# Kernel tuning notes

Hardware: AMD Instinct MI355X
Metric: run time of the kernel (lower is better)

The kernel has to match this reference:

```python
import jax, jax.numpy as jnp
import numpy as np

HEADS = 4
DIM_HEAD = 32
EPS = 1e-5


def setup_inputs() -> dict:
    key = jax.random.key(0)
    ks = jax.random.split(key, 3)
    b, c, h, w = 32, 128, 128, 128
    hidden = HEADS * DIM_HEAD  # 128
    x = jax.random.normal(ks[0], (b, c, h, w), dtype=jnp.float32)
    Wqkv = jax.random.normal(ks[1], (3 * hidden, c), dtype=jnp.float32) * (1.0 / np.sqrt(c))
    Wout = jax.random.normal(ks[2], (c, hidden), dtype=jnp.float32) * (1.0 / np.sqrt(hidden))
    bout = jnp.zeros((c,), dtype=jnp.float32)
    g = jnp.ones((c,), dtype=jnp.float32)
    return {"x": x, "Wqkv": Wqkv, "Wout": Wout, "bout": bout, "g": g}


def reference(x, Wqkv, Wout, bout, g):
    b, c, h, w = x.shape
    n = h * w
    scale = DIM_HEAD ** -0.5
    # 1x1 conv (no bias) == channel GEMM
    qkv = jnp.einsum('oc,bchw->bohw', Wqkv, x)  # [b, 3*hidden, h, w]
    q, k, v = jnp.split(qkv, 3, axis=1)
    # b (h d) x y -> b h d n
    def to_heads(t):
        return t.reshape(b, HEADS, DIM_HEAD, n)
    q, k, v = to_heads(q), to_heads(k), to_heads(v)
    q = jax.nn.softmax(q, axis=-2) * scale   # softmax over per-head channel dim
    k = jax.nn.softmax(k, axis=-1)           # softmax over token dim
    v = v / n
    ctx = jnp.einsum('bhdn,bhen->bhde', k, v)   # [b, heads, d, e]
    out = jnp.einsum('bhde,bhdn->bhen', ctx, q)  # [b, heads, e, n]
    out = out.reshape(b, HEADS * DIM_HEAD, h, w)
    # output 1x1 conv with bias
    y = jnp.einsum('oc,bchw->bohw', Wout, out) + bout[None, :, None, None]
    # LayerNorm over channel dim (biased variance)
    mean = jnp.mean(y, axis=1, keepdims=True)
    var = jnp.var(y, axis=1, keepdims=True)
    return (y - mean) * jax.lax.rsqrt(var + EPS) * g[None, :, None, None]
```

## Files before the change

### kernel.cpp

```cpp
#include <hip/hip_runtime.h>
#include <math.h>


#define NCHUNK 64

typedef __attribute__((ext_vector_type(8))) short short8;
typedef __attribute__((ext_vector_type(4))) float f32x4;

__device__ __forceinline__ uint bf16r(float f) {
    uint u = __float_as_uint(f);
    return (u + 0x7FFFu + ((u >> 16) & 1u)) >> 16;
}
__device__ __forceinline__ float bf16f(uint h) { return __uint_as_float(h << 16); }
__device__ __forceinline__ uint2 bsplit(float f) {
    uint h = bf16r(f);
    float r = f - bf16f(h);
    return make_uint2(h, bf16r(r));
}
__device__ __forceinline__ uint2 bsplit_t(float f) {
    uint u = __float_as_uint(f);
    uint uh = u & 0xFFFF0000u;
    float r = f - __uint_as_float(uh);
    return make_uint2(uh >> 16, __float_as_uint(r) >> 16);
}
__device__ __forceinline__ uint bpack_t(float f) {
    uint u = __float_as_uint(f);
    uint uh = u & 0xFFFF0000u;
    float r = f - __uint_as_float(uh);
    return (uh >> 16) | (__float_as_uint(r) & 0xFFFF0000u);
}
__device__ __forceinline__ short8 lo8(uint4 a, uint4 b) {
    uint4 r;
    r.x = (a.x & 0xFFFFu) | (a.y << 16);
    r.y = (a.z & 0xFFFFu) | (a.w << 16);
    r.z = (b.x & 0xFFFFu) | (b.y << 16);
    r.w = (b.z & 0xFFFFu) | (b.w << 16);
    return __builtin_bit_cast(short8, r);
}
__device__ __forceinline__ short8 hi8(uint4 a, uint4 b) {
    uint4 r;
    r.x = (a.x >> 16) | (a.y & 0xFFFF0000u);
    r.y = (a.z >> 16) | (a.w & 0xFFFF0000u);
    r.z = (b.x >> 16) | (b.y & 0xFFFF0000u);
    r.w = (b.z >> 16) | (b.w & 0xFFFF0000u);
    return __builtin_bit_cast(short8, r);
}

__global__ __launch_bounds__(256)
void wsplit(const float* __restrict__ W, ushort* __restrict__ Wh,
            ushort* __restrict__ Wl, int n)
{
    const int base = (blockIdx.x * 256 + threadIdx.x) * 4;
    if (base + 3 < n) {
        const float4 f = *(const float4*)(W + base);
        const uint2 a = bsplit(f.x), b2 = bsplit(f.y), c = bsplit(f.z), d = bsplit(f.w);
        ushort4 hh; hh.x = (ushort)a.x; hh.y = (ushort)b2.x; hh.z = (ushort)c.x; hh.w = (ushort)d.x;
        ushort4 ll; ll.x = (ushort)a.y; ll.y = (ushort)b2.y; ll.z = (ushort)c.y; ll.w = (ushort)d.y;
        *(ushort4*)(Wh + base) = hh;
        *(ushort4*)(Wl + base) = ll;
    }
}

#define MFMA(A, B, C) __builtin_amdgcn_mfma_f32_16x16x32_bf16((A), (B), (C), 0, 0, 0)

__global__ __launch_bounds__(512, 1)
void la_k1(const float* __restrict__ x,
           const ushort* __restrict__ Wh, const ushort* __restrict__ Wl,
           float* __restrict__ Spart, float* __restrict__ Zpart)
{
    __shared__ __align__(16) char smb[163840];

    const int tid = threadIdx.x;
    const int b = blockIdx.y, chunk = blockIdx.x;
    const int w = tid >> 6, l = tid & 63;
    const int l15 = l & 15, lg = l >> 4;

    {
#pragma unroll
        for (int it = 0; it < 16; ++it) {
            const int q = tid + 512 * it;
            const int region = q >> 12;
            const int lin = (q & 4095) * 16;
            const int r = lin >> 8;
            const int dst = (region << 16) + (lin ^ ((r & 7) << 4));
            const ushort* src = (region ? Wl : Wh) + 128 * 128 + (lin >> 1);
            *(uint4*)(&smb[dst]) = *(const uint4*)src;
        }
    }

    f32x4 s2[2];
#pragma unroll
    for (int i = 0; i < 2; ++i) s2[i] = (f32x4){0.f, 0.f, 0.f, 0.f};
    float zrow[4];
#pragma unroll
    for (int i = 0; i < 4; ++i) zrow[i] = 0.f;

    const int hh = w >> 1, eh = w & 1;

    for (int t = 0; t < 8; ++t) {
        const int p0 = chunk * 256 + t * 32;
        {
            const float* xb = x + (size_t)b * 128 * 16384 + p0;
            const int cp = tid >> 3, j = tid & 7;
            const int pb = j * 4, c = cp * 2;
            const float4 a = *(const float4*)(xb + (size_t)c * 16384 + pb);
            const float4 bq = *(const float4*)(xb + (size_t)(c + 1) * 16384 + pb);
            const float av[4] = {a.x, a.y, a.z, a.w};
            const float bv[4] = {bq.x, bq.y, bq.z, bq.w};
#pragma unroll
            for (int pp = 0; pp < 4; ++pp) {
                const uint2 s0 = bsplit_t(av[pp]);
                const uint2 s1 = bsplit_t(bv[pp]);
                const int p = pb + pp;
                const int byt = (p * 256 + c * 2) ^ (((p ^ (p >> 3)) & 7) << 4);
                *(uint*)(&smb[131072 + byt])        = s0.x | (s1.x << 16);
                *(uint*)(&smb[131072 + 8192 + byt]) = s0.y | (s1.y << 16);
            }
        }
        __syncthreads();

        f32x4 acc[2][2];
#pragma unroll
        for (int rt = 0; rt < 2; ++rt)
#pragma unroll
            for (int ct = 0; ct < 2; ++ct) acc[rt][ct] = (f32x4){0.f, 0.f, 0.f, 0.f};
#pragma unroll
        for (int ks = 0; ks < 4; ++ks) {
            short8 Bh[2], Bl[2];
#pragma unroll
            for (int ct = 0; ct < 2; ++ct) {
                const int p = ct * 16 + l15;
                const int byt = (p * 256 + (ks * 32 + lg * 8) * 2) ^ (((p ^ (p >> 3)) & 7) << 4);
                Bh[ct] = *(const short8*)(&smb[131072 + byt]);
                Bl[ct] = *(const short8*)(&smb[131072 + 8192 + byt]);
            }
#pragma unroll
            for (int rt = 0; rt < 2; ++rt) {
                const int r = (w + rt * 8) * 16 + l15;
                const int abyt = (r * 256 + (ks * 32 + lg * 8) * 2) ^ ((r & 7) << 4);
                const short8 Ah_ = *(const short8*)(&smb[abyt]);
                const short8 Al_ = *(const short8*)(&smb[65536 + abyt]);
#pragma unroll
                for (int ct = 0; ct < 2; ++ct) {
                    acc[rt][ct] = MFMA(Ah_, Bh[ct], acc[rt][ct]);
                    acc[rt][ct] = MFMA(Ah_, Bl[ct], acc[rt][ct]);
                    acc[rt][ct] = MFMA(Al_, Bh[ct], acc[rt][ct]);
                }
            }
        }
        __syncthreads();

#pragma unroll
        for (int rt = 0; rt < 2; ++rt) {
            const bool isk = (rt == 0);
#pragma unroll
            for (int ct = 0; ct < 2; ++ct) {
                const int p = ct * 16 + l15;
#pragma unroll
                for (int i = 0; i < 4; ++i) {
                    float val = acc[rt][ct][i];
                    if (isk) {
                        val = expf(val);
                        zrow[i] += val;
                    }
                    const int r = w * 16 + lg * 4 + i;
                    const int byt = (r * 128 + p * 4) ^ ((r & 7) << 4);
                    *(uint*)(&smb[131072 + (isk ? 0 : 16384) + byt]) = bpack_t(val);
                }
            }
        }
        __syncthreads();

        {
            short8 A2h[2], A2l[2], B2h, B2l;
#pragma unroll
            for (int rt2 = 0; rt2 < 2; ++rt2) {
                const int r = hh * 32 + rt2 * 16 + l15;
                const int b0 = (r * 128 + lg * 32) ^ ((r & 7) << 4);
                const int b1 = (r * 128 + lg * 32 + 16) ^ ((r & 7) << 4);
                const uint4 q0 = *(const uint4*)(&smb[131072 + b0]);
                const uint4 q1 = *(const uint4*)(&smb[131072 + b1]);
                A2h[rt2] = lo8(q0, q1);
                A2l[rt2] = hi8(q0, q1);
            }
            {
                const int rv = hh * 32 + eh * 16 + l15;
                const int c0 = (rv * 128 + lg * 32) ^ ((rv & 7) << 4);
                const int c1 = (rv * 128 + lg * 32 + 16) ^ ((rv & 7) << 4);
                const uint4 r0 = *(const uint4*)(&smb[131072 + 16384 + c0]);
                const uint4 r1 = *(const uint4*)(&smb[131072 + 16384 + c1]);
                B2h = lo8(r0, r1);
                B2l = hi8(r0, r1);
            }
#pragma unroll
            for (int rt2 = 0; rt2 < 2; ++rt2) {
                s2[rt2] = MFMA(A2h[rt2], B2h, s2[rt2]);
                s2[rt2] = MFMA(A2h[rt2], B2l, s2[rt2]);
                s2[rt2] = MFMA(A2l[rt2], B2h, s2[rt2]);
            }
        }
        __syncthreads();
    }

    const size_t sbase = (((size_t)b * NCHUNK + chunk) * 4 + hh) * 1024;
#pragma unroll
    for (int rt2 = 0; rt2 < 2; ++rt2)
#pragma unroll
        for (int i = 0; i < 4; ++i) {
            const int d = rt2 * 16 + lg * 4 + i;
            const int e = eh * 16 + l15;
            Spart[sbase + d * 32 + e] = s2[rt2][i];
        }

#pragma unroll
    for (int i = 0; i < 4; ++i) {
        float z = zrow[i];
        z += __shfl_xor(z, 1, 64);
        z += __shfl_xor(z, 2, 64);
        z += __shfl_xor(z, 4, 64);
        z += __shfl_xor(z, 8, 64);
        if (l15 == 0)
            Zpart[((size_t)b * NCHUNK + chunk) * 128 + w * 16 + lg * 4 + i] = z;
    }
}

__global__ __launch_bounds__(256, 1)
void la_k1_reduce(const float* __restrict__ Spart, const float* __restrict__ Zpart,
                  float* __restrict__ ctxF)
{
    const int tid = threadIdx.x;
    const int b  = blockIdx.x >> 2;
    const int hh = blockIdx.x & 3;
    const int d  = tid >> 3;
    const int e0 = (tid & 7) << 2;
    float sx = 0.f, sy = 0.f, sz = 0.f, sw = 0.f, z = 0.f;
    for (int ch = 0; ch < NCHUNK; ++ch) {
        const size_t base = (((size_t)b * NCHUNK + ch) * 4 + hh) * 32 + d;
        const float4 v = *(const float4*)(Spart + base * 32 + e0);
        sx += v.x; sy += v.y; sz += v.z; sw += v.w;
        z += Zpart[base];
    }
    const float inv = 1.0f / (z * 16384.0f);
    float4 r; r.x = sx * inv; r.y = sy * inv; r.z = sz * inv; r.w = sw * inv;
    *(float4*)(ctxF + ((((size_t)b * 4 + hh) * 32 + d) << 5) + e0) = r;
}

__global__ __launch_bounds__(256, 1)
void la_mk(const float* __restrict__ Wout, const float* __restrict__ ctxF,
           ushort* __restrict__ Mh, ushort* __restrict__ Ml)
{
    __shared__ float ctxs[4096];
    const int b = blockIdx.x;
    const int tid = threadIdx.x;
#pragma unroll
    for (int i = 0; i < 4; ++i) {
        const int idx = (tid + 256 * i) * 4;
        *(float4*)(ctxs + idx) = *(const float4*)(ctxF + (size_t)b * 4096 + idx);
    }
    __syncthreads();
    const int cp = tid & 127;
    const int dh = tid >> 7;
#pragma unroll
    for (int hq = 0; hq < 2; ++hq) {
        const int h = dh * 2 + hq;
        float wrow[32];
#pragma unroll
        for (int e4 = 0; e4 < 8; ++e4) {
            const float4 wv = *(const float4*)(Wout + cp * 128 + h * 32 + e4 * 4);
            wrow[e4 * 4 + 0] = wv.x; wrow[e4 * 4 + 1] = wv.y;
            wrow[e4 * 4 + 2] = wv.z; wrow[e4 * 4 + 3] = wv.w;
        }
        for (int d = 0; d < 32; ++d) {
            float m = 0.f;
#pragma unroll
            for (int e = 0; e < 32; ++e)
                m += wrow[e] * ctxs[h * 1024 + d * 32 + e];
            const uint2 s = bsplit(m);
            const size_t mo = (size_t)b * 16384 + cp * 128 + h * 32 + d;
            Mh[mo] = (ushort)s.x;
            Ml[mo] = (ushort)s.y;
        }
    }
}

__device__ __forceinline__ int xswz64(int p, int cbyte) {
    return (p * 256 + cbyte) ^ (((p ^ (p >> 3)) & 7) << 4);
}
__device__ __forceinline__ int qswz(int p, int off) {
    return (p * 64 + off) ^ (((p >> 1) & 3) << 4);
}

__global__ __launch_bounds__(256, 4)
void la_k2(const float* __restrict__ x,
           const ushort* __restrict__ Wqh, const ushort* __restrict__ Wql,
           const ushort* __restrict__ Mh, const ushort* __restrict__ Ml,
           const float* __restrict__ bout, const float* __restrict__ g,
           float* __restrict__ outg)
{
    __shared__ __align__(16) char smb[32768];

    const int tid = threadIdx.x;
    const int b = blockIdx.y, chunk = blockIdx.x;
    const int p0 = chunk * 64;
    const int w = tid >> 6, l = tid & 63;
    const int l15 = l & 15, lg = l >> 4;
    const int ch2 = w >> 1;
    const int rp  = w & 1;

    short8 AqH[2][4], AqL[2][4];
#pragma unroll
    for (int t_ = 0; t_ < 2; ++t_)
#pragma unroll
        for (int ks = 0; ks < 4; ++ks) {
            const size_t aoff = (size_t)((2 * w + t_) * 16 + l15) * 128 + ks * 32 + lg * 8;
            AqH[t_][ks] = *(const short8*)(Wqh + aoff);
            AqL[t_][ks] = *(const short8*)(Wql + aoff);
        }

    {
        const float* xb = x + (size_t)b * 128 * 16384 + p0;
        const int j = tid & 15, gq = tid >> 4;
        const int pb = j * 4;
#pragma unroll
        for (int u = 0; u < 2; ++u) {
            const int cb = gq * 4 + u * 64;
            const float4 xv0 = *(const float4*)(xb + (size_t)(cb + 0) * 16384 + pb);
            const float4 xv1 = *(const float4*)(xb + (size_t)(cb + 1) * 16384 + pb);
            const float4 xv2 = *(const float4*)(xb + (size_t)(cb + 2) * 16384 + pb);
            const float4 xv3 = *(const float4*)(xb + (size_t)(cb + 3) * 16384 + pb);
            float rc[4][4];
            rc[0][0] = xv0.x; rc[0][1] = xv0.y; rc[0][2] = xv0.z; rc[0][3] = xv0.w;
            rc[1][0] = xv1.x; rc[1][1] = xv1.y; rc[1][2] = xv1.z; rc[1][3] = xv1.w;
            rc[2][0] = xv2.x; rc[2][1] = xv2.y; rc[2][2] = xv2.z; rc[2][3] = xv2.w;
            rc[3][0] = xv3.x; rc[3][1] = xv3.y; rc[3][2] = xv3.z; rc[3][3] = xv3.w;
#pragma unroll
            for (int pp = 0; pp < 4; ++pp) {
                const uint2 s0 = bsplit_t(rc[0][pp]);
                const uint2 s1 = bsplit_t(rc[1][pp]);
                const uint2 s2u = bsplit_t(rc[2][pp]);
                const uint2 s3 = bsplit_t(rc[3][pp]);
                const int p = pb + pp;
                const int byt = xswz64(p, cb * 2);
                *(uint2*)(&smb[byt])         = make_uint2(s0.x | (s1.x << 16), s2u.x | (s3.x << 16));
                *(uint2*)(&smb[16384 + byt]) = make_uint2(s0.y | (s1.y << 16), s2u.y | (s3.y << 16));
            }
        }
    }
    __syncthreads();

    f32x4 qacc[2][4];
#pragma unroll
    for (int t_ = 0; t_ < 2; ++t_)
#pragma unroll
        for (int ct = 0; ct < 4; ++ct) qacc[t_][ct] = (f32x4){0.f, 0.f, 0.f, 0.f};
#pragma unroll
    for (int ks = 0; ks < 4; ++ks) {
#pragma unroll
        for (int ct = 0; ct < 4; ++ct) {
            const int p = ct * 16 + l15;
            const int byt = xswz64(p, (ks * 32 + lg * 8) * 2);
            const short8 Bh_ = *(const short8*)(&smb[byt]);
            const short8 Bl_ = *(const short8*)(&smb[16384 + byt]);
#pragma unroll
            for (int t_ = 0; t_ < 2; ++t_) {
                qacc[t_][ct] = MFMA(AqH[t_][ks], Bh_, qacc[t_][ct]);
                qacc[t_][ct] = MFMA(AqH[t_][ks], Bl_, qacc[t_][ct]);
                qacc[t_][ct] = MFMA(AqL[t_][ks], Bh_, qacc[t_][ct]);
            }
        }
    }

    float vv[4][2][4];
#pragma unroll
    for (int ct = 0; ct < 4; ++ct) {
        float s = 0.f;
#pragma unroll
        for (int t_ = 0; t_ < 2; ++t_)
#pragma unroll
            for (int i = 0; i < 4; ++i) {
                vv[ct][t_][i] = expf(qacc[t_][ct][i]);
                s += vv[ct][t_][i];
            }
        s += __shfl_xor(s, 16, 64);
        s += __shfl_xor(s, 32, 64);
        const float inv = 0.17677669529663687f / s;
#pragma unroll
        for (int t_ = 0; t_ < 2; ++t_)
#pragma unroll
            for (int i = 0; i < 4; ++i) vv[ct][t_][i] *= inv;
    }
    __syncthreads();

#pragma unroll
    for (int ct = 0; ct < 4; ++ct) {
        const int p = ct * 16 + l15;
#pragma unroll
        for (int t_ = 0; t_ < 2; ++t_) {
            const uint2 a0 = bsplit_t(vv[ct][t_][0]);
            const uint2 a1 = bsplit_t(vv[ct][t_][1]);
            const uint2 a2 = bsplit_t(vv[ct][t_][2]);
            const uint2 a3 = bsplit_t(vv[ct][t_][3]);
            const int byt = w * 4096 + qswz(p, (t_ * 16 + lg * 4) * 2);
            *(uint2*)(&smb[byt])         = make_uint2(a0.x | (a1.x << 16), a2.x | (a3.x << 16));
            *(uint2*)(&smb[16384 + byt]) = make_uint2(a0.y | (a1.y << 16), a2.y | (a3.y << 16));
        }
    }
    __syncthreads();

    f32x4 yacc[4][2];
#pragma unroll
    for (int jj = 0; jj < 4; ++jj)
#pragma unroll
        for (int ct = 0; ct < 2; ++ct) yacc[jj][ct] = (f32x4){0.f, 0.f, 0.f, 0.f};
#pragma unroll
    for (int ks = 0; ks < 4; ++ks) {
        short8 Bh[2], Bl[2];
#pragma unroll
        for (int ct = 0; ct < 2; ++ct) {
            const int p = ch2 * 32 + ct * 16 + l15;
            const int byt = ks * 4096 + qswz(p, lg * 16);
            Bh[ct] = *(const short8*)(&smb[byt]);
            Bl[ct] = *(const short8*)(&smb[16384 + byt]);
        }
#pragma unroll
        for (int jj = 0; jj < 4; ++jj) {
            const int T = rp + 2 * jj;
            const size_t aoff = (size_t)b * 16384 + (size_t)(T * 16 + l15) * 128 + ks * 32 + lg * 8;
            const short8 Ah_ = *(const short8*)(Mh + aoff);
            const short8 Al_ = *(const short8*)(Ml + aoff);
#pragma unroll
            for (int ct = 0; ct < 2; ++ct) {
                yacc[jj][ct] = MFMA(Ah_, Bh[ct], yacc[jj][ct]);
                yacc[jj][ct] = MFMA(Ah_, Bl[ct], yacc[jj][ct]);
                yacc[jj][ct] = MFMA(Al_, Bh[ct], yacc[jj][ct]);
            }
        }
    }
    __syncthreads();

    float4 bo[4], gv[4];
#pragma unroll
    for (int jj = 0; jj < 4; ++jj) {
        const int rbase = (rp + 2 * jj) * 16 + lg * 4;
        bo[jj] = *(const float4*)(bout + rbase);
        gv[jj] = *(const float4*)(g + rbase);
    }
#pragma unroll
    for (int jj = 0; jj < 4; ++jj)
#pragma unroll
        for (int ct = 0; ct < 2; ++ct) {
            yacc[jj][ct][0] += bo[jj].x;
            yacc[jj][ct][1] += bo[jj].y;
            yacc[jj][ct][2] += bo[jj].z;
            yacc[jj][ct][3] += bo[jj].w;
        }
    float* lnred = (float*)smb;
    float sm[2], sq[2];
#pragma unroll
    for (int ct = 0; ct < 2; ++ct) {
        float s = 0.f, q = 0.f;
#pragma unroll
        for (int jj = 0; jj < 4; ++jj)
#pragma unroll
            for (int i = 0; i < 4; ++i) {
                const float yv = yacc[jj][ct][i];
                s += yv; q += yv * yv;
            }
        s += __shfl_xor(s, 16, 64); q += __shfl_xor(q, 16, 64);
        s += __shfl_xor(s, 32, 64); q += __shfl_xor(q, 32, 64);
        sm[ct] = s; sq[ct] = q;
    }
    if (lg == 0) {
#pragma unroll
        for (int ct = 0; ct < 2; ++ct) {
            const int p = ch2 * 32 + ct * 16 + l15;
            lnred[(p * 2 + rp) * 2 + 0] = sm[ct];
            lnred[(p * 2 + rp) * 2 + 1] = sq[ct];
        }
    }
    __syncthreads();
#pragma unroll
    for (int ct = 0; ct < 2; ++ct) {
        const int p = ch2 * 32 + ct * 16 + l15;
        const float st = lnred[(p * 2 + 0) * 2 + 0] + lnred[(p * 2 + 1) * 2 + 0];
        const float qt = lnred[(p * 2 + 0) * 2 + 1] + lnred[(p * 2 + 1) * 2 + 1];
        const float mean = st * (1.0f / 128.0f);
        const float var  = qt * (1.0f / 128.0f) - mean * mean;
        const float rstd = 1.0f / sqrtf(var + 1e-5f);
#pragma unroll
        for (int jj = 0; jj < 4; ++jj) {
            const int rbase = (rp + 2 * jj) * 16 + lg * 4;
            const float gg[4] = {gv[jj].x, gv[jj].y, gv[jj].z, gv[jj].w};
#pragma unroll
            for (int i = 0; i < 4; ++i) {
                const float val = (yacc[jj][ct][i] - mean) * rstd * gg[i];
                outg[((size_t)b * 128 + rbase + i) * 16384 + p0 + p] = val;
            }
        }
    }
}

extern "C" void kernel_launch(void* const* d_in, const int* in_sizes, int n_in,
                              void* d_out, int out_size, void* d_ws, size_t ws_size,
                              hipStream_t stream) {
    const float* x    = (const float*)d_in[0];
    const float* Wqkv = (const float*)d_in[1];
    const float* Wout = (const float*)d_in[2];
    const float* bout = (const float*)d_in[3];
    const float* g    = (const float*)d_in[4];
    float* out = (float*)d_out;

    float* Spart = (float*)d_ws;
    float* Zpart = Spart + (size_t)32 * NCHUNK * 4 * 32 * 32;
    float* ctxF  = Zpart + (size_t)32 * NCHUNK * 4 * 32;
    ushort* Wqh  = (ushort*)(ctxF + (size_t)32 * 4096);
    ushort* Wql  = Wqh + 384 * 128;
    ushort* Mh   = (ushort*)Spart;
    ushort* Ml   = Mh + (size_t)32 * 16384;
    (void)in_sizes; (void)n_in; (void)out_size; (void)ws_size;

    wsplit<<<dim3(48), 256, 0, stream>>>(Wqkv, Wqh, Wql, 384 * 128);
    la_k1<<<dim3(NCHUNK, 32), 512, 0, stream>>>(x, Wqh, Wql, Spart, Zpart);
    la_k1_reduce<<<dim3(128), 256, 0, stream>>>(Spart, Zpart, ctxF);
    la_mk<<<dim3(32), 256, 0, stream>>>(Wout, ctxF, Mh, Ml);
    la_k2<<<dim3(256, 32), 256, 0, stream>>>(x, Wqh, Wql, Mh, Ml, bout, g, out);
}
```

Measured before the change: 470.0 us.

## Make output kernel persistent with weights staged once in LDS

Result: faster. 452.7 us (median of 2 runs) (-3.7%).

```diff
diff --git a/kernel.cpp b/kernel.cpp
--- a/kernel.cpp
+++ b/kernel.cpp
@@ -290,40 +290,47 @@
     return (p * 64 + off) ^ (((p >> 1) & 3) << 4);
 }
 
-__global__ __launch_bounds__(256, 4)
-void la_k2(const float* __restrict__ x,
-           const ushort* __restrict__ Wqh, const ushort* __restrict__ Wql,
-           const ushort* __restrict__ Mh, const ushort* __restrict__ Ml,
-           const float* __restrict__ bout, const float* __restrict__ g,
-           float* __restrict__ outg)
+__global__ __launch_bounds__(512, 1)
+void la_k2s(const float* __restrict__ x,
+            const ushort* __restrict__ Wqh, const ushort* __restrict__ Wql,
+            const ushort* __restrict__ Mh, const ushort* __restrict__ Ml,
+            const float* __restrict__ bout, const float* __restrict__ g,
+            float* __restrict__ outg)
 {
-    __shared__ __align__(16) char smb[32768];
+    __shared__ __align__(16) char smb[163840];
 
     const int tid = threadIdx.x;
-    const int b = blockIdx.y, chunk = blockIdx.x;
-    const int p0 = chunk * 64;
+    const int b = blockIdx.y, blk = blockIdx.x;
     const int w = tid >> 6, l = tid & 63;
     const int l15 = l & 15, lg = l >> 4;
-    const int ch2 = w >> 1;
-    const int rp  = w & 1;
-
-    short8 AqH[2][4], AqL[2][4];
-#pragma unroll
-    for (int t_ = 0; t_ < 2; ++t_)
-#pragma unroll
-        for (int ks = 0; ks < 4; ++ks) {
-            const size_t aoff = (size_t)((2 * w + t_) * 16 + l15) * 128 + ks * 32 + lg * 8;
-            AqH[t_][ks] = *(const short8*)(Wqh + aoff);
-            AqL[t_][ks] = *(const short8*)(Wql + aoff);
-        }
+    const int hq = w >> 1, ph = w & 1;
 
     {
-        const float* xb = x + (size_t)b * 128 * 16384 + p0;
-        const int j = tid & 15, gq = tid >> 4;
-        const int pb = j * 4;
-#pragma unroll
-        for (int u = 0; u < 2; ++u) {
-            const int cb = gq * 4 + u * 64;
+        const ushort* mhb = Mh + (size_t)b * 16384;
+        const ushort* mlb = Ml + (size_t)b * 16384;
+#pragma unroll
+        for (int it = 0; it < 16; ++it) {
+            const int q = tid + 512 * it;
+            const int plane = q >> 11;
+            const int lin = (q & 2047) * 16;
+            const int r = lin >> 8;
+            const int dst = plane * 32768 + (lin ^ ((r & 7) << 4));
+            const ushort* src = (plane == 0 ? Wqh : plane == 1 ? Wql
+                               : plane == 2 ? mhb : mlb) + (lin >> 1);
+            *(uint4*)(&smb[dst]) = *(const uint4*)src;
+        }
+    }
+
+    const float4 bo = *(const float4*)(bout + w * 16 + lg * 4);
+    const float4 gv = *(const float4*)(g + w * 16 + lg * 4);
+
+    for (int it = 0; it < 32; ++it) {
+        const int p0 = blk * 2048 + it * 64;
+
+        {
+            const float* xb = x + (size_t)b * 128 * 16384 + p0;
+            const int j = tid & 15, gq = tid >> 4;
+            const int pb = j * 4, cb = gq * 4;
             const float4 xv0 = *(const float4*)(xb + (size_t)(cb + 0) * 16384 + pb);
             const float4 xv1 = *(const float4*)(xb + (size_t)(cb + 1) * 16384 + pb);
             const float4 xv2 = *(const float4*)(xb + (size_t)(cb + 2) * 16384 + pb);
@@ -341,162 +348,145 @@
                 const uint2 s3 = bsplit_t(rc[3][pp]);
                 const int p = pb + pp;
                 const int byt = xswz64(p, cb * 2);
-                *(uint2*)(&smb[byt])         = make_uint2(s0.x | (s1.x << 16), s2u.x | (s3.x << 16));
-                *(uint2*)(&smb[16384 + byt]) = make_uint2(s0.y | (s1.y << 16), s2u.y | (s3.y << 16));
-            }
-        }
-    }
-    __syncthreads();
-
-    f32x4 qacc[2][4];
-#pragma unroll
-    for (int t_ = 0; t_ < 2; ++t_)
-#pragma unroll
-        for (int ct = 0; ct < 4; ++ct) qacc[t_][ct] = (f32x4){0.f, 0.f, 0.f, 0.f};
-#pragma unroll
-    for (int ks = 0; ks < 4; ++ks) {
+                *(uint2*)(&smb[131072 + byt]) = make_uint2(s0.x | (s1.x << 16), s2u.x | (s3.x << 16));
+                *(uint2*)(&smb[147456 + byt]) = make_uint2(s0.y | (s1.y << 16), s2u.y | (s3.y << 16));
+            }
+        }
+        __syncthreads();
+
+        f32x4 qacc[2][2];
+#pragma unroll
+        for (int t_ = 0; t_ < 2; ++t_)
+#pragma unroll
+            for (int ct = 0; ct < 2; ++ct) qacc[t_][ct] = (f32x4){0.f, 0.f, 0.f, 0.f};
+#pragma unroll
+        for (int ks = 0; ks < 4; ++ks) {
+            short8 Bh[2], Bl[2];
+#pragma unroll
+            for (int ct = 0; ct < 2; ++ct) {
+                const int p = ph * 32 + ct * 16 + l15;
+                const int byt = xswz64(p, (ks * 32 + lg * 8) * 2);
+                Bh[ct] = *(const short8*)(&smb[131072 + byt]);
+                Bl[ct] = *(const short8*)(&smb[147456 + byt]);
+            }
+#pragma unroll
+            for (int t_ = 0; t_ < 2; ++t_) {
+                const int r = hq * 32 + t_ * 16 + l15;
+                const int abyt = (r * 256 + (ks * 32 + lg * 8) * 2) ^ ((r & 7) << 4);
+                const short8 Ah_ = *(const short8*)(&smb[abyt]);
+                const short8 Al_ = *(const short8*)(&smb[32768 + abyt]);
+#pragma unroll
+                for (int ct = 0; ct < 2; ++ct) {
+                    qacc[t_][ct] = MFMA(Ah_, Bh[ct], qacc[t_][ct]);
+                    qacc[t_][ct] = MFMA(Ah_, Bl[ct], qacc[t_][ct]);
+                    qacc[t_][ct] = MFMA(Al_, Bh[ct], qacc[t_][ct]);
+                }
+            }
+        }
+
+        float vv[2][2][4];
+#pragma unroll
+        for (int ct = 0; ct < 2; ++ct) {
+            float s = 0.f;
+#pragma unroll
+            for (int t_ = 0; t_ < 2; ++t_)
+#pragma unroll
+                for (int i = 0; i < 4; ++i) {
+                    vv[ct][t_][i] = expf(qacc[t_][ct][i]);
+                    s += vv[ct][t_][i];
+                }
+            s += __shfl_xor(s, 16, 64);
+            s += __shfl_xor(s, 32, 64);
+            const float inv = 0.17677669529663687f / s;
+#pragma unroll
+            for (int t_ = 0; t_ < 2; ++t_)
+#pragma unroll
+                for (int i = 0; i < 4; ++i) vv[ct][t_][i] *= inv;
+        }
+        __syncthreads();
+
+#pragma unroll
+        for (int ct = 0; ct < 2; ++ct) {
+            const int p = ph * 32 + ct * 16 + l15;
+#pragma unroll
+            for (int t_ = 0; t_ < 2; ++t_) {
+                const uint2 a0 = bsplit_t(vv[ct][t_][0]);
+                const uint2 a1 = bsplit_t(vv[ct][t_][1]);
+                const uint2 a2 = bsplit_t(vv[ct][t_][2]);
+                const uint2 a3 = bsplit_t(vv[ct][t_][3]);
+                const int byt = hq * 4096 + qswz(p, (t_ * 16 + lg * 4) * 2);
+                *(uint2*)(&smb[131072 + byt]) = make_uint2(a0.x | (a1.x << 16), a2.x | (a3.x << 16));
+                *(uint2*)(&smb[147456 + byt]) = make_uint2(a0.y | (a1.y << 16), a2.y | (a3.y << 16));
+            }
+        }
+        __syncthreads();
+
+        f32x4 yacc[4];
+#pragma unroll
+        for (int ct = 0; ct < 4; ++ct) yacc[ct] = (f32x4){0.f, 0.f, 0.f, 0.f};
+#pragma unroll
+        for (int ks = 0; ks < 4; ++ks) {
+            const int r = w * 16 + l15;
+            const int abyt = (r * 256 + (ks * 32 + lg * 8) * 2) ^ ((r & 7) << 4);
+            const short8 Ah_ = *(const short8*)(&smb[65536 + abyt]);
+            const short8 Al_ = *(const short8*)(&smb[98304 + abyt]);
+#pragma unroll
+            for (int ct = 0; ct < 4; ++ct) {
+                const int p = ct * 16 + l15;
+                const int byt = ks * 4096 + qswz(p, lg * 16);
+                const short8 Bh_ = *(const short8*)(&smb[131072 + byt]);
+                const short8 Bl_ = *(const short8*)(&smb[147456 + byt]);
+                yacc[ct] = MFMA(Ah_, Bh_, yacc[ct]);
+                yacc[ct] = MFMA(Ah_, Bl_, yacc[ct]);
+                yacc[ct] = MFMA(Al_, Bh_, yacc[ct]);
+            }
+        }
+        __syncthreads();
+
+#pragma unroll
+        for (int ct = 0; ct < 4; ++ct) {
+            yacc[ct][0] += bo.x; yacc[ct][1] += bo.y;
+            yacc[ct][2] += bo.z; yacc[ct][3] += bo.w;
+        }
+        float* lnred = (float*)(smb + 131072);
+#pragma unroll
+        for (int ct = 0; ct < 4; ++ct) {
+            float s = 0.f, q = 0.f;
+#pragma unroll
+            for (int i = 0; i < 4; ++i) {
+                const float yv = yacc[ct][i];
+                s += yv; q += yv * yv;
+            }
+            s += __shfl_xor(s, 16, 64); q += __shfl_xor(q, 16, 64);
+            s += __shfl_xor(s, 32, 64); q += __shfl_xor(q, 32, 64);
+            if (lg == 0) {
+                const int p = ct * 16 + l15;
+                lnred[(p * 8 + w) * 2 + 0] = s;
+                lnred[(p * 8 + w) * 2 + 1] = q;
+            }
+        }
+        __syncthreads();
 #pragma unroll
         for (int ct = 0; ct < 4; ++ct) {
             const int p = ct * 16 + l15;
-            const int byt = xswz64(p, (ks * 32 + lg * 8) * 2);
-            const short8 Bh_ = *(const short8*)(&smb[byt]);
-            const short8 Bl_ = *(const short8*)(&smb[16384 + byt]);
-#pragma unroll
-            for (int t_ = 0; t_ < 2; ++t_) {
-                qacc[t_][ct] = MFMA(AqH[t_][ks], Bh_, qacc[t_][ct]);
-                qacc[t_][ct] = MFMA(AqH[t_][ks], Bl_, qacc[t_][ct]);
-                qacc[t_][ct] = MFMA(AqL[t_][ks], Bh_, qacc[t_][ct]);
-            }
-        }
-    }
-
-    float vv[4][2][4];
-#pragma unroll
-    for (int ct = 0; ct < 4; ++ct) {
-        float s = 0.f;
-#pragma unroll
-        for (int t_ = 0; t_ < 2; ++t_)
+            float st = 0.f, qt = 0.f;
+#pragma unroll
+            for (int ww = 0; ww < 8; ++ww) {
+                st += lnred[(p * 8 + ww) * 2 + 0];
+                qt += lnred[(p * 8 + ww) * 2 + 1];
+            }
+            const float mean = st * (1.0f / 128.0f);
+            const float var  = qt * (1.0f / 128.0f) - mean * mean;
+            const float rstd = 1.0f / sqrtf(var + 1e-5f);
+            const float gg[4] = {gv.x, gv.y, gv.z, gv.w};
 #pragma unroll
             for (int i = 0; i < 4; ++i) {
-                vv[ct][t_][i] = expf(qacc[t_][ct][i]);
-                s += vv[ct][t_][i];
-            }
-        s += __shfl_xor(s, 16, 64);
-        s += __shfl_xor(s, 32, 64);
-        const float inv = 0.17677669529663687f / s;
-#pragma unroll
-        for (int t_ = 0; t_ < 2; ++t_)
-#pragma unroll
-            for (int i = 0; i < 4; ++i) vv[ct][t_][i] *= inv;
-    }
-    __syncthreads();
-
-#pragma unroll
-    for (int ct = 0; ct < 4; ++ct) {
-        const int p = ct * 16 + l15;
-#pragma unroll
-        for (int t_ = 0; t_ < 2; ++t_) {
-            const uint2 a0 = bsplit_t(vv[ct][t_][0]);
-            const uint2 a1 = bsplit_t(vv[ct][t_][1]);
-            const uint2 a2 = bsplit_t(vv[ct][t_][2]);
-            const uint2 a3 = bsplit_t(vv[ct][t_][3]);
-            const int byt = w * 4096 + qswz(p, (t_ * 16 + lg * 4) * 2);
-            *(uint2*)(&smb[byt])         = make_uint2(a0.x | (a1.x << 16), a2.x | (a3.x << 16));
-            *(uint2*)(&smb[16384 + byt]) = make_uint2(a0.y | (a1.y << 16), a2.y | (a3.y << 16));
-        }
-    }
-    __syncthreads();
-
-    f32x4 yacc[4][2];
-#pragma unroll
-    for (int jj = 0; jj < 4; ++jj)
-#pragma unroll
-        for (int ct = 0; ct < 2; ++ct) yacc[jj][ct] = (f32x4){0.f, 0.f, 0.f, 0.f};
-#pragma unroll
-    for (int ks = 0; ks < 4; ++ks) {
-        short8 Bh[2], Bl[2];
-#pragma unroll
-        for (int ct = 0; ct < 2; ++ct) {
-            const int p = ch2 * 32 + ct * 16 + l15;
-            const int byt = ks * 4096 + qswz(p, lg * 16);
-            Bh[ct] = *(const short8*)(&smb[byt]);
-            Bl[ct] = *(const short8*)(&smb[16384 + byt]);
-        }
-#pragma unroll
-        for (int jj = 0; jj < 4; ++jj) {
-            const int T = rp + 2 * jj;
-            const size_t aoff = (size_t)b * 16384 + (size_t)(T * 16 + l15) * 128 + ks * 32 + lg * 8;
-            const short8 Ah_ = *(const short8*)(Mh + aoff);
-            const short8 Al_ = *(const short8*)(Ml + aoff);
-#pragma unroll
-            for (int ct = 0; ct < 2; ++ct) {
-                yacc[jj][ct] = MFMA(Ah_, Bh[ct], yacc[jj][ct]);
-                yacc[jj][ct] = MFMA(Ah_, Bl[ct], yacc[jj][ct]);
-                yacc[jj][ct] = MFMA(Al_, Bh[ct], yacc[jj][ct]);
-            }
-        }
-    }
-    __syncthreads();
-
-    float4 bo[4], gv[4];
-#pragma unroll
-    for (int jj = 0; jj < 4; ++jj) {
-        const int rbase = (rp + 2 * jj) * 16 + lg * 4;
-        bo[jj] = *(const float4*)(bout + rbase);
-        gv[jj] = *(const float4*)(g + rbase);
-    }
-#pragma unroll
-    for (int jj = 0; jj < 4; ++jj)
-#pragma unroll
-        for (int ct = 0; ct < 2; ++ct) {
-            yacc[jj][ct][0] += bo[jj].x;
-            yacc[jj][ct][1] += bo[jj].y;
-            yacc[jj][ct][2] += bo[jj].z;
-            yacc[jj][ct][3] += bo[jj].w;
-        }
-    float* lnred = (float*)smb;
-    float sm[2], sq[2];
-#pragma unroll
-    for (int ct = 0; ct < 2; ++ct) {
-        float s = 0.f, q = 0.f;
-#pragma unroll
-        for (int jj = 0; jj < 4; ++jj)
-#pragma unroll
-            for (int i = 0; i < 4; ++i) {
-                const float yv = yacc[jj][ct][i];
-                s += yv; q += yv * yv;
-            }
-        s += __shfl_xor(s, 16, 64); q += __shfl_xor(q, 16, 64);
-        s += __shfl_xor(s, 32, 64); q += __shfl_xor(q, 32, 64);
-        sm[ct] = s; sq[ct] = q;
-    }
-    if (lg == 0) {
-#pragma unroll
-        for (int ct = 0; ct < 2; ++ct) {
-            const int p = ch2 * 32 + ct * 16 + l15;
-            lnred[(p * 2 + rp) * 2 + 0] = sm[ct];
-            lnred[(p * 2 + rp) * 2 + 1] = sq[ct];
-        }
-    }
-    __syncthreads();
-#pragma unroll
-    for (int ct = 0; ct < 2; ++ct) {
-        const int p = ch2 * 32 + ct * 16 + l15;
-        const float st = lnred[(p * 2 + 0) * 2 + 0] + lnred[(p * 2 + 1) * 2 + 0];
-        const float qt = lnred[(p * 2 + 0) * 2 + 1] + lnred[(p * 2 + 1) * 2 + 1];
-        const float mean = st * (1.0f / 128.0f);
-        const float var  = qt * (1.0f / 128.0f) - mean * mean;
-        const float rstd = 1.0f / sqrtf(var + 1e-5f);
-#pragma unroll
-        for (int jj = 0; jj < 4; ++jj) {
-            const int rbase = (rp + 2 * jj) * 16 + lg * 4;
-            const float gg[4] = {gv[jj].x, gv[jj].y, gv[jj].z, gv[jj].w};
-#pragma unroll
-            for (int i = 0; i < 4; ++i) {
-                const float val = (yacc[jj][ct][i] - mean) * rstd * gg[i];
-                outg[((size_t)b * 128 + rbase + i) * 16384 + p0 + p] = val;
-            }
-        }
+                const int o = w * 16 + lg * 4 + i;
+                outg[((size_t)b * 128 + o) * 16384 + p0 + p] =
+                    (yacc[ct][i] - mean) * rstd * gg[i];
+            }
+        }
+        __syncthreads();
     }
 }
 
@@ -523,5 +513,5 @@
     la_k1<<<dim3(NCHUNK, 32), 512, 0, stream>>>(x, Wqh, Wql, Spart, Zpart);
     la_k1_reduce<<<dim3(128), 256, 0, stream>>>(Spart, Zpart, ctxF);
     la_mk<<<dim3(32), 256, 0, stream>>>(Wout, ctxF, Mh, Ml);
-    la_k2<<<dim3(256, 32), 256, 0, stream>>>(x, Wqh, Wql, Mh, Ml, bout, g, out);
-}
+    la_k2s<<<dim3(8, 32), 512, 0, stream>>>(x, Wqh, Wql, Mh, Ml, bout, g, out);
+}
```
